# Performance work log

Measured on AMD Instinct MI355X. Metric: run time of the kernel, lower is better.

Reference implementation:

```python
import jax, jax.numpy as jnp
import numpy as np

# Model constants (from init_kwargs)
NF, NC, E, B = 100000, 4000, 500000, 256
D_FACT, D_COMP = 1536, 27
HIDDEN, HEADS, CPH = 128, 4, 32  # out_per_head = hidden // heads
NUM_LAYERS = 2
TIME_DIM = 8
T_SCALE = 30.0
EDGE_DIM = 2 + TIME_DIM  # [sentiment, decay, time2vec]
ATTN_SCALE = 1.0  # 1 / attn_temperature
NEG_SLOPE = 0.2


def time_edge_features(ea, lam):
    # ea: [E, 2] = [sentiment, decay]; second column in [0,1] -> decay branch
    s = jnp.clip(ea[:, 0:1], -1.0, 1.0)
    decay = jnp.clip(ea[:, 1:2], 0.0, 1.0)
    lam = jnp.maximum(lam, 1e-6)
    delta_t = -jnp.log(jnp.maximum(decay, 1e-6)) / lam
    t = jnp.log1p(jnp.maximum(delta_t, 0.0)) / T_SCALE  # [E,1]
    freqs = jnp.arange(1, TIME_DIM, dtype=ea.dtype)      # [TIME_DIM-1]
    sins = jnp.sin(t * freqs)                            # [E,TIME_DIM-1]
    return jnp.concatenate([s, decay, sins, t], axis=-1)  # [E, EDGE_DIM]


def seg_softmax(logits, seg, n):
    # logits: [E,H]; softmax over edges sharing the same destination node
    m = jax.ops.segment_max(logits, seg, num_segments=n)
    z = jnp.exp(logits - m[seg])
    den = jax.ops.segment_sum(z, seg, num_segments=n)
    return z / (den[seg] + 1e-16)


def seg_mean(x, seg, n):
    s = jax.ops.segment_sum(x, seg, num_segments=n)
    cnt = jax.ops.segment_sum(jnp.ones((x.shape[0],), x.dtype), seg, num_segments=n)
    return s / jnp.maximum(cnt, 1.0)[:, None]


def layernorm(x, g, b, eps=1e-5):
    mu = jnp.mean(x, axis=-1, keepdims=True)
    var = jnp.var(x, axis=-1, keepdims=True)
    return (x - mu) * jax.lax.rsqrt(var + eps) * g + b


def setup_inputs() -> dict:
    key = jax.random.key(0)
    ks = jax.random.split(key, 32)

    x_fact = jax.random.normal(ks[0], (NF, D_FACT), jnp.float32)
    x_company = jax.random.normal(ks[1], (NC, D_COMP), jnp.float32)
    u = jax.random.uniform(ks[2], (E, 2), jnp.float32)
    edge_attr = jnp.concatenate([u[:, 0:1] * 2.0 - 1.0, u[:, 1:2]], axis=1)
    edge_index = jnp.stack([
        jax.random.randint(ks[3], (E,), 0, NF),
        jax.random.randint(ks[4], (E,), 0, NC),
    ]).astype(jnp.int32)
    batch_fact = jnp.sort(jax.random.randint(ks[5], (NF,), 0, B)).astype(jnp.int32)
    batch_company = jnp.sort(jax.random.randint(ks[6], (NC,), 0, B)).astype(jnp.int32)

    def p(k, shape):
        return jax.random.normal(k, shape, jnp.float32) * 0.05

    inp = dict(
        x_fact=x_fact, x_company=x_company, edge_attr=edge_attr,
        edge_index=edge_index, batch_fact=batch_fact, batch_company=batch_company,
        lambda_decay=jnp.array(0.01, jnp.float32),
        Wf=p(ks[7], (D_FACT, HIDDEN)), bf=jnp.zeros((HIDDEN,), jnp.float32),
        Wc=p(ks[8], (D_COMP, HIDDEN)), bc=jnp.zeros((HIDDEN,), jnp.float32),
        Wl=p(ks[9], (NUM_LAYERS, HIDDEN, HIDDEN)), bl=jnp.zeros((NUM_LAYERS, HIDDEN), jnp.float32),
        Wr=p(ks[10], (NUM_LAYERS, HIDDEN, HIDDEN)), br=jnp.zeros((NUM_LAYERS, HIDDEN), jnp.float32),
        We=p(ks[11], (NUM_LAYERS, EDGE_DIM, HIDDEN)), be=jnp.zeros((NUM_LAYERS, HIDDEN), jnp.float32),
        att=p(ks[12], (NUM_LAYERS, HEADS, CPH)),
        bias_out=jnp.zeros((NUM_LAYERS, HIDDEN), jnp.float32),
        ln_g=jnp.ones((NUM_LAYERS, HIDDEN), jnp.float32), ln_b=jnp.zeros((NUM_LAYERS, HIDDEN), jnp.float32),
        Wg=p(ks[13], (2 * HIDDEN, 1)), bg=jnp.zeros((1,), jnp.float32),
        W1=p(ks[14], (HIDDEN, HIDDEN)), b1=jnp.zeros((HIDDEN,), jnp.float32),
        W2=p(ks[15], (HIDDEN, 1)), b2=jnp.zeros((1,), jnp.float32),
    )
    return inp


def reference(x_fact, x_company, edge_attr, edge_index, batch_fact, batch_company,
              lambda_decay, Wf, bf, Wc, bc, Wl, bl, Wr, br, We, be, att, bias_out,
              ln_g, ln_b, Wg, bg, W1, b1, W2, b2):
    src, dst = edge_index[0], edge_index[1]
    ef = time_edge_features(edge_attr, lambda_decay)          # [E, EDGE_DIM]

    # per-node-type input encoders
    hf = jax.nn.relu(x_fact @ Wf + bf)                         # [NF, H]
    hc = jax.nn.relu(x_company @ Wc + bc)                      # [NC, H]
    n_c = x_company.shape[0]

    for l in range(NUM_LAYERS):
        # GATv2 (edge-conditioned, bipartite fact->company, share_weights=False)
        gl = (hf @ Wl[l] + bl[l]).reshape(-1, HEADS, CPH)      # src transform [NF,H,C]
        gr = (hc @ Wr[l] + br[l]).reshape(-1, HEADS, CPH)      # dst transform [NC,H,C]
        ge = (ef @ We[l] + be[l]).reshape(-1, HEADS, CPH)      # edge transform [E,H,C]
        e = jax.nn.leaky_relu(gl[src] + gr[dst] + ge, NEG_SLOPE)  # [E,H,C]
        logits = jnp.einsum('ehc,hc->eh', e, att[l]) * ATTN_SCALE  # [E,H]
        alpha = seg_softmax(logits, dst, n_c)                   # scatter-softmax over dst
        msg = alpha[..., None] * gl[src]                        # [E,H,C]
        out = jax.ops.segment_sum(msg, dst, num_segments=n_c).reshape(n_c, HIDDEN) + bias_out[l]
        hc = layernorm(hc + jax.nn.relu(out), ln_g[l], ln_b[l])  # residual + post-norm

    # gated readout over graphs in batch
    pf = seg_mean(hf, batch_fact, B)                            # [B,H]
    pc = seg_mean(hc, batch_company, B)                         # [B,H]
    g = jax.nn.sigmoid(jnp.concatenate([pf, pc], axis=-1) @ Wg + bg)  # [B,1]
    h = g * pf + (1.0 - g) * pc                                 # [B,H]
    logit = jax.nn.relu(h @ W1 + b1) @ W2 + b2                  # [B,1]
    return logit
```

## Files before the change

### kernel.cpp

```cpp
#include <hip/hip_runtime.h>
#include <hip/hip_bf16.h>
#include <math.h>

#define NFAC 100000
#define NCOMP 4000
#define NEDGE 500000
#define NB 256
#define DF 1536
#define DC 27
#define H 128
#define EDIM 10
#define EDIMP 16

typedef __attribute__((ext_vector_type(8))) short short8v;
typedef __attribute__((ext_vector_type(4))) float f32x4;

#define GLOAD_LDS16(g, l)                                                              \
  __builtin_amdgcn_global_load_lds((const __attribute__((address_space(1))) unsigned int*)(g), \
                                   (__attribute__((address_space(3))) unsigned int*)(l), 16, 0, 0)

__device__ __forceinline__ float group32_sum(float v) {
#pragma unroll
  for (int m = 16; m > 0; m >>= 1) v += __shfl_xor(v, m);
  return v;
}

__device__ __forceinline__ unsigned short bf16rn(float x) {
  unsigned int u = __float_as_uint(x);
  unsigned int r = (u + 0x7fffu + ((u >> 16) & 1u)) >> 16;
  return (unsigned short)r;
}
__device__ __forceinline__ float bf16tof(unsigned short h) {
  return __uint_as_float(((unsigned int)h) << 16);
}

__global__ void k_edge_feat(const float* __restrict__ ea, const float* __restrict__ lamp,
                            float* __restrict__ ef) {
  int e = blockIdx.x * blockDim.x + threadIdx.x;
  if (e >= NEDGE) return;
  float s   = fminf(fmaxf(ea[2 * e], -1.f), 1.f);
  float dec = fminf(fmaxf(ea[2 * e + 1], 0.f), 1.f);
  float lam = fmaxf(lamp[0], 1e-6f);
  float dt  = -logf(fmaxf(dec, 1e-6f)) / lam;
  float t   = log1pf(fmaxf(dt, 0.f)) * (1.f / 30.f);
  float* o = ef + (size_t)e * EDIMP;
  o[0] = s;
  o[1] = dec;
#pragma unroll
  for (int k = 1; k < 8; k++) o[1 + k] = __sinf(t * (float)k);
  o[9] = t;
  o[10] = 0.f; o[11] = 0.f; o[12] = 0.f; o[13] = 0.f; o[14] = 0.f; o[15] = 0.f;
}

__global__ void k_hist(const int* __restrict__ dst, int* __restrict__ deg) {
  int e = blockIdx.x * blockDim.x + threadIdx.x;
  if (e < NEDGE) atomicAdd(&deg[dst[e]], 1);
}

__global__ __launch_bounds__(1024) void k_scan(const int* __restrict__ deg, int* __restrict__ off) {
  __shared__ int s[4096];
  int t = threadIdx.x;
  for (int i = t; i < 4096; i += 1024) s[i] = (i < NCOMP) ? deg[i] : 0;
  __syncthreads();
  for (int d = 1; d < 4096; d <<= 1) {
    int vals[4];
#pragma unroll
    for (int j = 0; j < 4; j++) {
      int i = t + j * 1024;
      vals[j] = (i >= d) ? s[i - d] : 0;
    }
    __syncthreads();
#pragma unroll
    for (int j = 0; j < 4; j++) {
      int i = t + j * 1024;
      s[i] += vals[j];
    }
    __syncthreads();
  }
  for (int i = t; i < 4096; i += 1024) off[i + 1] = s[i];
  if (t == 0) off[0] = 0;
}

__global__ void k_scatter(const int* __restrict__ dst, const int* __restrict__ src,
                          const int* __restrict__ off, int* __restrict__ cur,
                          int* __restrict__ eid, int* __restrict__ srcs) {
  int e = blockIdx.x * blockDim.x + threadIdx.x;
  if (e < NEDGE) {
    int d = dst[e];
    int p = atomicAdd(&cur[d], 1);
    eid[off[d] + p] = e;
    srcs[off[d] + p] = src[e];
  }
}

__global__ void k_conv_w(const float* __restrict__ W, unsigned short* __restrict__ Bh,
                         unsigned short* __restrict__ Bl, int K) {
  int i = blockIdx.x * blockDim.x + threadIdx.x;
  if (i >= K * H) return;
  int k = i >> 7, c = i & 127;
  float x = W[i];
  unsigned short h = bf16rn(x);
  unsigned short l = bf16rn(x - bf16tof(h));
  Bh[(size_t)c * K + k] = h;
  Bl[(size_t)c * K + k] = l;
}

__global__ void k_conv_wl2(const float* __restrict__ Wl, unsigned short* __restrict__ Bh,
                           unsigned short* __restrict__ Bl) {
  int i = blockIdx.x * blockDim.x + threadIdx.x;
  if (i >= 2 * H * H) return;
  int l = i >> 14;
  int r = i & 16383;
  int k = r >> 7, c = r & 127;
  float x = Wl[i];
  unsigned short h = bf16rn(x);
  unsigned short lo = bf16rn(x - bf16tof(h));
  int col = c + 128 * l;
  Bh[(size_t)col * H + k] = h;
  Bl[(size_t)col * H + k] = lo;
}

__device__ __forceinline__ unsigned int packhi(unsigned int u1, unsigned int u0) {
  return __builtin_amdgcn_perm(u1, u0, 0x07060302u);
}

__device__ __forceinline__ void split8(const float4& a0, const float4& a1, short8v& ah,
                                       short8v& al) {
  float xs[8] = {a0.x, a0.y, a0.z, a0.w, a1.x, a1.y, a1.z, a1.w};
  unsigned int hu[8], lu[8];
#pragma unroll
  for (int j = 0; j < 8; j++) {
    unsigned int u = __float_as_uint(xs[j]);
    hu[j] = u & 0xffff0000u;
    lu[j] = __float_as_uint(xs[j] - __uint_as_float(hu[j]));
  }
  unsigned int hw[4], lw[4];
#pragma unroll
  for (int j = 0; j < 4; j++) {
    hw[j] = packhi(hu[2 * j + 1], hu[2 * j]);
    lw[j] = packhi(lu[2 * j + 1], lu[2 * j]);
  }
  ah = *(short8v*)hw;
  al = *(short8v*)lw;
}

__global__ __launch_bounds__(256, 2) void k_gemm_mfma(const float* __restrict__ A,
                                                      const unsigned short* __restrict__ Bth,
                                                      const unsigned short* __restrict__ Btl,
                                                      const float* __restrict__ bias,
                                                      float* __restrict__ C, int M, int K,
                                                      int dorelu, float* __restrict__ Cpart) {
  __shared__ __align__(16) char smem[2][32768];
  int tid = threadIdx.x;
  int wave = tid >> 6, lane = tid & 63;
  int m0 = blockIdx.x * 128;
  int wm = (wave >> 1) * 64, wn = (wave & 1) * 64;
  int fr = lane & 15, fg = lane >> 4;
  int nsplit = gridDim.y;
  int Ks = K / nsplit;
  int kbeg = blockIdx.y * Ks;
  int nIter = Ks >> 5;

  f32x4 acc[4][4];
#pragma unroll
  for (int i = 0; i < 4; i++)
#pragma unroll
    for (int j = 0; j < 4; j++) acc[i][j] = (f32x4){0.f, 0.f, 0.f, 0.f};

  int a_row = (lane >> 3);
  int a_s = lane & 7;
  int b_col = (lane >> 2);
  int b_s = lane & 3;

  auto stage = [&](int buf, int k0) {
    char* base = smem[buf];
#pragma unroll
    for (int q = 0; q < 4; q++) {
      int j = wave + 4 * q;
      int row = j * 8 + a_row;
      int grow = m0 + row;
      if (grow >= M) grow = 0;
      const float* src = A + (size_t)grow * K + k0 + ((a_s ^ (row & 7)) << 2);
      GLOAD_LDS16(src, base + j * 1024);
    }
#pragma unroll
    for (int q = 0; q < 2; q++) {
      int j = wave + 4 * q;
      int col = j * 16 + b_col;
      int soff = k0 + ((b_s ^ (col & 3)) << 3);
      GLOAD_LDS16(Bth + (size_t)col * K + soff, base + 16384 + j * 1024);
      GLOAD_LDS16(Btl + (size_t)col * K + soff, base + 24576 + j * 1024);
    }
  };

  stage(0, kbeg);
  __syncthreads();

  for (int it = 0; it < nIter; ++it) {
    int cur = it & 1;
    if (it + 1 < nIter) stage(cur ^ 1, kbeg + ((it + 1) << 5));
    const char* cb = smem[cur];
    short8v ah[4], al[4];
#pragma unroll
    for (int mf = 0; mf < 4; mf++) {
      int r = wm + 16 * mf + fr;
      int s0 = (2 * fg) ^ (r & 7);
      int s1 = (2 * fg + 1) ^ (r & 7);
      float4 a0 = *(const float4*)(cb + r * 128 + s0 * 16);
      float4 a1 = *(const float4*)(cb + r * 128 + s1 * 16);
      split8(a0, a1, ah[mf], al[mf]);
    }
#pragma unroll
    for (int nf = 0; nf < 4; nf++) {
      int c = wn + 16 * nf + fr;
      int sb = fg ^ (c & 3);
      short8v bh = *(const short8v*)(cb + 16384 + c * 64 + sb * 16);
      short8v bl = *(const short8v*)(cb + 24576 + c * 64 + sb * 16);
#pragma unroll
      for (int mf = 0; mf < 4; mf++) {
        acc[mf][nf] = __builtin_amdgcn_mfma_f32_16x16x32_bf16(ah[mf], bh, acc[mf][nf], 0, 0, 0);
        acc[mf][nf] = __builtin_amdgcn_mfma_f32_16x16x32_bf16(ah[mf], bl, acc[mf][nf], 0, 0, 0);
        acc[mf][nf] = __builtin_amdgcn_mfma_f32_16x16x32_bf16(al[mf], bh, acc[mf][nf], 0, 0, 0);
      }
    }
    __syncthreads();
  }

  if (nsplit == 1) {
#pragma unroll
    for (int mf = 0; mf < 4; mf++) {
      int rbase = m0 + wm + 16 * mf + 4 * fg;
#pragma unroll
      for (int nf = 0; nf < 4; nf++) {
        int col = wn + 16 * nf + fr;
        float bv = bias[col];
#pragma unroll
        for (int j = 0; j < 4; j++) {
          int row = rbase + j;
          if (row < M) {
            float v = acc[mf][nf][j] + bv;
            if (dorelu) v = fmaxf(v, 0.f);
            C[(size_t)row * H + col] = v;
          }
        }
      }
    }
  } else {
    float* P = Cpart + (size_t)blockIdx.y * M * H;
#pragma unroll
    for (int mf = 0; mf < 4; mf++) {
      int rbase = m0 + wm + 16 * mf + 4 * fg;
#pragma unroll
      for (int nf = 0; nf < 4; nf++) {
        int col = wn + 16 * nf + fr;
#pragma unroll
        for (int j = 0; j < 4; j++) {
          int row = rbase + j;
          if (row < M) P[(size_t)row * H + col] = acc[mf][nf][j];
        }
      }
    }
  }
}

__global__ __launch_bounds__(256, 2) void k_gemm_n256(const float* __restrict__ A,
                                                      const unsigned short* __restrict__ Bth,
                                                      const unsigned short* __restrict__ Btl,
                                                      const float* __restrict__ bias,
                                                      float* __restrict__ C, int M) {
  __shared__ __align__(16) char smem[2][40960];
  const int K = 128;
  int tid = threadIdx.x;
  int wave = tid >> 6, lane = tid & 63;
  int m0 = blockIdx.x * 64;
  int wn = wave * 64;
  int fr = lane & 15, fg = lane >> 4;

  f32x4 acc[4][4];
#pragma unroll
  for (int i = 0; i < 4; i++)
#pragma unroll
    for (int j = 0; j < 4; j++) acc[i][j] = (f32x4){0.f, 0.f, 0.f, 0.f};

  int a_row = (lane >> 3);
  int a_s = lane & 7;
  int b_col = (lane >> 2);
  int b_s = lane & 3;

  auto stage = [&](int buf, int k0) {
    char* base = smem[buf];
#pragma unroll
    for (int q = 0; q < 2; q++) {
      int j = wave + 4 * q;
      int row = j * 8 + a_row;
      int grow = m0 + row;
      if (grow >= M) grow = 0;
      GLOAD_LDS16(A + (size_t)grow * K + k0 + ((a_s ^ (row & 7)) << 2), base + j * 1024);
    }
#pragma unroll
    for (int q = 0; q < 4; q++) {
      int j = wave + 4 * q;
      int col = j * 16 + b_col;
      int soff = k0 + ((b_s ^ (col & 3)) << 3);
      GLOAD_LDS16(Bth + (size_t)col * K + soff, base + 8192 + j * 1024);
      GLOAD_LDS16(Btl + (size_t)col * K + soff, base + 24576 + j * 1024);
    }
  };

  stage(0, 0);
  __syncthreads();

  for (int it = 0; it < 4; ++it) {
    int cur = it & 1;
    if (it + 1 < 4) stage(cur ^ 1, (it + 1) << 5);
    const char* cb = smem[cur];
    short8v ah[4], al[4];
#pragma unroll
    for (int mf = 0; mf < 4; mf++) {
      int r = 16 * mf + fr;
      int s0 = (2 * fg) ^ (r & 7);
      int s1 = (2 * fg + 1) ^ (r & 7);
      float4 a0 = *(const float4*)(cb + r * 128 + s0 * 16);
      float4 a1 = *(const float4*)(cb + r * 128 + s1 * 16);
      split8(a0, a1, ah[mf], al[mf]);
    }
#pragma unroll
    for (int nf = 0; nf < 4; nf++) {
      int c = wn + 16 * nf + fr;
      int sb = fg ^ (c & 3);
      short8v bh = *(const short8v*)(cb + 8192 + c * 64 + sb * 16);
      short8v bl = *(const short8v*)(cb + 24576 + c * 64 + sb * 16);
#pragma unroll
      for (int mf = 0; mf < 4; mf++) {
        acc[mf][nf] = __builtin_amdgcn_mfma_f32_16x16x32_bf16(ah[mf], bh, acc[mf][nf], 0, 0, 0);
        acc[mf][nf] = __builtin_amdgcn_mfma_f32_16x16x32_bf16(ah[mf], bl, acc[mf][nf], 0, 0, 0);
        acc[mf][nf] = __builtin_amdgcn_mfma_f32_16x16x32_bf16(al[mf], bh, acc[mf][nf], 0, 0, 0);
      }
    }
    __syncthreads();
  }

#pragma unroll
  for (int mf = 0; mf < 4; mf++) {
    int rbase = m0 + 16 * mf + 4 * fg;
#pragma unroll
    for (int nf = 0; nf < 4; nf++) {
      int col = wn + 16 * nf + fr;
      float bv = bias[col];
#pragma unroll
      for (int j = 0; j < 4; j++) {
        int row = rbase + j;
        if (row < M) C[(size_t)row * 256 + col] = acc[mf][nf][j] + bv;
      }
    }
  }
}

__global__ __launch_bounds__(256) void k_reduce2(const float* __restrict__ P0,
                                                 const float* __restrict__ P1,
                                                 const float* __restrict__ bias,
                                                 float* __restrict__ C, int total4) {
  int i = blockIdx.x * blockDim.x + threadIdx.x;
  if (i >= total4) return;
  float4 a = ((const float4*)P0)[i];
  float4 b = ((const float4*)P1)[i];
  float4 bv = ((const float4*)bias)[i & 31];
  float4 r;
  r.x = fmaxf(a.x + b.x + bv.x, 0.f);
  r.y = fmaxf(a.y + b.y + bv.y, 0.f);
  r.z = fmaxf(a.z + b.z + bv.z, 0.f);
  r.w = fmaxf(a.w + b.w + bv.w, 0.f);
  ((float4*)C)[i] = r;
}

__global__ void k_enc_comp(const float* __restrict__ X, const float* __restrict__ Wc,
                           const float* __restrict__ bc, float* __restrict__ hc) {
  int tid = threadIdx.x;
  int r = blockIdx.x * 2 + (tid >> 7);
  int j = tid & 127;
  if (r >= NCOMP) return;
  float acc = bc[j];
  const float* x = X + (size_t)r * DC;
#pragma unroll
  for (int k = 0; k < DC; k++) acc = fmaf(x[k], Wc[k * H + j], acc);
  hc[(size_t)r * H + j] = fmaxf(acc, 0.f);
}

__global__ __launch_bounds__(128) void k_node(
    const float* __restrict__ gl, const float* __restrict__ ef, const int* __restrict__ srcs,
    const int* __restrict__ csr_off, const int* __restrict__ csr_eid,
    const float* __restrict__ Wr, const float* __restrict__ br, const float* __restrict__ We,
    const float* __restrict__ be, const float* __restrict__ att,
    const float* __restrict__ bias_out, const float* __restrict__ lng,
    const float* __restrict__ lnb, float* __restrict__ hc) {
  int v = blockIdx.x;
  int t = threadIdx.x;
  __shared__ float hcs[H];
  __shared__ float red[2], redq[2];
  float x = hc[(size_t)v * H + t];
  hcs[t] = x;
  float wre[EDIM];
#pragma unroll
  for (int k = 0; k < EDIM; k++) wre[k] = We[k * H + t];
  float attv = att[t];
  float bev = be[t];
  __syncthreads();
  float grv = br[t];
  for (int k = 0; k < H; k++) grv = fmaf(hcs[k], Wr[k * H + t], grv);
  float grb = grv + bev;

  int e0 = csr_off[v], e1 = csr_off[v + 1];
  float m = -INFINITY, s = 0.f, acc = 0.f;
  int i = e0;
  float glv = 0.f;
  float4 f0 = {0, 0, 0, 0}, f1 = {0, 0, 0, 0};
  float2 f2 = {0, 0};
  if (i < e1) {
    int eid = csr_eid[i];
    int sid = srcs[i];
    glv = gl[(size_t)sid * 256 + t];
    const float* efr = ef + (size_t)eid * EDIMP;
    f0 = *(const float4*)(efr);
    f1 = *(const float4*)(efr + 4);
    f2 = *(const float2*)(efr + 8);
  }
  while (i < e1) {
    int ni = i + 1;
    float nglv = 0.f;
    float4 nf0 = {0, 0, 0, 0}, nf1 = {0, 0, 0, 0};
    float2 nf2 = {0, 0};
    if (ni < e1) {
      int eid = csr_eid[ni];
      int sid = srcs[ni];
      nglv = gl[(size_t)sid * 256 + t];
      const float* efr = ef + (size_t)eid * EDIMP;
      nf0 = *(const float4*)(efr);
      nf1 = *(const float4*)(efr + 4);
      nf2 = *(const float2*)(efr + 8);
    }
    float ge = grb;
    ge = fmaf(f0.x, wre[0], ge);
    ge = fmaf(f0.y, wre[1], ge);
    ge = fmaf(f0.z, wre[2], ge);
    ge = fmaf(f0.w, wre[3], ge);
    ge = fmaf(f1.x, wre[4], ge);
    ge = fmaf(f1.y, wre[5], ge);
    ge = fmaf(f1.z, wre[6], ge);
    ge = fmaf(f1.w, wre[7], ge);
    ge = fmaf(f2.x, wre[8], ge);
    ge = fmaf(f2.y, wre[9], ge);
    float ev = glv + ge;
    ev = ev > 0.f ? ev : 0.2f * ev;
    float logit = group32_sum(ev * attv);
    if (logit > m) {
      float scale = __expf(m - logit);
      s = s * scale + 1.f;
      acc = acc * scale + glv;
      m = logit;
    } else {
      float z = __expf(logit - m);
      s += z;
      acc = fmaf(z, glv, acc);
    }
    glv = nglv;
    f0 = nf0;
    f1 = nf1;
    f2 = nf2;
    i = ni;
  }
  float outv = acc / (s + 1e-16f);
  outv += bias_out[t];
  outv = fmaxf(outv, 0.f);
  float y = x + outv;
  float sv = y, qv = y * y;
#pragma unroll
  for (int mm = 32; mm > 0; mm >>= 1) {
    sv += __shfl_xor(sv, mm);
    qv += __shfl_xor(qv, mm);
  }
  int wid = t >> 6, lane = t & 63;
  if (lane == 0) {
    red[wid] = sv;
    redq[wid] = qv;
  }
  __syncthreads();
  float mean = (red[0] + red[1]) * (1.f / H);
  float var = (redq[0] + redq[1]) * (1.f / H) - mean * mean;
  float r = rsqrtf(var + 1e-5f);
  hc[(size_t)v * H + t] = (y - mean) * r * lng[t] + lnb[t];
}

template <int CHUNK>
__global__ __launch_bounds__(128) void k_segmean(const float* __restrict__ X,
                                                 const int* __restrict__ seg, int n,
                                                 float* __restrict__ sum, int* __restrict__ cnt) {
  int t = threadIdx.x;
  int n0 = blockIdx.x * CHUNK;
  int n1 = min(n0 + CHUNK, n);
  float acc = 0.f;
  int c = 0;
  int curs = -1;
  for (int i = n0; i < n1; ++i) {
    int sg = seg[i];
    if (sg != curs) {
      if (curs >= 0) {
        atomicAdd(&sum[(size_t)curs * H + t], acc);
        if (t == 0) atomicAdd(&cnt[curs], c);
      }
      curs = sg;
      acc = 0.f;
      c = 0;
    }
    acc += X[(size_t)i * H + t];
    c++;
  }
  if (curs >= 0) {
    atomicAdd(&sum[(size_t)curs * H + t], acc);
    if (t == 0) atomicAdd(&cnt[curs], c);
  }
}

__global__ __launch_bounds__(128) void k_readout(const float* __restrict__ pf,
                                                 const float* __restrict__ pc,
                                                 const int* __restrict__ cf,
                                                 const int* __restrict__ cc,
                                                 const float* __restrict__ Wg,
                                                 const float* __restrict__ bg,
                                                 const float* __restrict__ W1,
                                                 const float* __restrict__ b1,
                                                 const float* __restrict__ W2,
                                                 const float* __restrict__ b2,
                                                 float* __restrict__ out) {
  int b = blockIdx.x, t = threadIdx.x;
  __shared__ float hs[H];
  __shared__ float red[2], red2[2];
  int wid = t >> 6, lane = t & 63;
  float nf = fmaxf((float)cf[b], 1.f);
  float nc = fmaxf((float)cc[b], 1.f);
  float pfv = pf[(size_t)b * H + t] / nf;
  float pcv = pc[(size_t)b * H + t] / nc;
  float gp = pfv * Wg[t] + pcv * Wg[H + t];
  float sv = gp;
#pragma unroll
  for (int mm = 32; mm > 0; mm >>= 1) sv += __shfl_xor(sv, mm);
  if (lane == 0) red[wid] = sv;
  __syncthreads();
  float g = 1.f / (1.f + expf(-(red[0] + red[1] + bg[0])));
  float h = g * pfv + (1.f - g) * pcv;
  hs[t] = h;
  __syncthreads();
  float a = b1[t];
  for (int k = 0; k < H; k++) a = fmaf(hs[k], W1[k * H + t], a);
  a = fmaxf(a, 0.f);
  float p = a * W2[t];
#pragma unroll
  for (int mm = 32; mm > 0; mm >>= 1) p += __shfl_xor(p, mm);
  if (lane == 0) red2[wid] = p;
  __syncthreads();
  if (t == 0) out[b] = red2[0] + red2[1] + b2[0];
}

extern "C" void kernel_launch(void* const* d_in, const int* in_sizes, int n_in, void* d_out,
                              int out_size, void* d_ws, size_t ws_size, hipStream_t stream) {
  const float* x_fact = (const float*)d_in[0];
  const float* x_comp = (const float*)d_in[1];
  const float* ea = (const float*)d_in[2];
  const int* eidx = (const int*)d_in[3];
  const int* batf = (const int*)d_in[4];
  const int* batc = (const int*)d_in[5];
  const float* lam = (const float*)d_in[6];
  const float* Wf = (const float*)d_in[7];
  const float* bf = (const float*)d_in[8];
  const float* Wc = (const float*)d_in[9];
  const float* bc = (const float*)d_in[10];
  const float* Wl = (const float*)d_in[11];
  const float* bl = (const float*)d_in[12];
  const float* Wr = (const float*)d_in[13];
  const float* br_ = (const float*)d_in[14];
  const float* We = (const float*)d_in[15];
  const float* be = (const float*)d_in[16];
  const float* att = (const float*)d_in[17];
  const float* b_out = (const float*)d_in[18];
  const float* lng = (const float*)d_in[19];
  const float* lnb = (const float*)d_in[20];
  const float* Wg = (const float*)d_in[21];
  const float* bg = (const float*)d_in[22];
  const float* W1 = (const float*)d_in[23];
  const float* b1 = (const float*)d_in[24];
  const float* W2 = (const float*)d_in[25];
  const float* b2 = (const float*)d_in[26];
  float* out = (float*)d_out;

  char* w = (char*)d_ws;
  auto carve = [&](size_t bytes) -> char* {
    char* p = w;
    w += (bytes + 255) & ~(size_t)255;
    return p;
  };
  float* HF = (float*)carve((size_t)NFAC * H * 4);
  float* GL = (float*)carve((size_t)NFAC * H * 4);
  float* CP1 = (float*)carve((size_t)NFAC * H * 4);
  float* GL2 = GL;
  float* HC = (float*)carve((size_t)NCOMP * H * 4);
  float* EF = (float*)carve((size_t)NEDGE * EDIMP * 4);
  int* OFF = (int*)carve(4100 * 4);
  int* EID = (int*)carve((size_t)NEDGE * 4);
  int* SRCS = (int*)carve((size_t)NEDGE * 4);
  unsigned short* WfH = (unsigned short*)carve((size_t)DF * H * 2);
  unsigned short* WfL = (unsigned short*)carve((size_t)DF * H * 2);
  unsigned short* WlH2 = (unsigned short*)carve((size_t)256 * H * 2);
  unsigned short* WlL2 = (unsigned short*)carve((size_t)256 * H * 2);
  char* zbase = w;
  int* DEG = (int*)carve(4096 * 4);
  int* CUR = (int*)carve(4096 * 4);
  float* PF = (float*)carve((size_t)NB * H * 4);
  float* PC = (float*)carve((size_t)NB * H * 4);
  int* CF = (int*)carve(NB * 4);
  int* CC = (int*)carve(NB * 4);
  size_t zbytes = (size_t)(w - zbase);
  hipMemsetAsync(zbase, 0, zbytes, stream);

  const int* srcArr = eidx;
  const int* dstArr = eidx + NEDGE;

  k_edge_feat<<<(NEDGE + 255) / 256, 256, 0, stream>>>(ea, lam, EF);
  k_hist<<<(NEDGE + 255) / 256, 256, 0, stream>>>(dstArr, DEG);
  k_scan<<<1, 1024, 0, stream>>>(DEG, OFF);
  k_scatter<<<(NEDGE + 255) / 256, 256, 0, stream>>>(dstArr, srcArr, OFF, CUR, EID, SRCS);

  k_conv_w<<<(DF * H + 255) / 256, 256, 0, stream>>>(Wf, WfH, WfL, DF);
  k_conv_wl2<<<(2 * H * H + 255) / 256, 256, 0, stream>>>(Wl, WlH2, WlL2);

  {
    float* CPART = GL;
    dim3 grid((NFAC + 127) / 128, 2);
    k_gemm_mfma<<<grid, 256, 0, stream>>>(x_fact, WfH, WfL, bf, HF, NFAC, DF, 1, CPART);
    int total4 = NFAC * H / 4;
    k_reduce2<<<(total4 + 255) / 256, 256, 0, stream>>>(GL, CP1, bf, HF, total4);
  }
  k_enc_comp<<<NCOMP / 2, 256, 0, stream>>>(x_comp, Wc, bc, HC);

  k_gemm_n256<<<(NFAC + 63) / 64, 256, 0, stream>>>(HF, WlH2, WlL2, bl, GL2, NFAC);

  for (int l = 0; l < 2; l++) {
    k_node<<<NCOMP, 128, 0, stream>>>(GL2 + l * 128, EF, SRCS, OFF, EID,
                                      Wr + (size_t)l * H * H, br_ + l * H,
                                      We + (size_t)l * EDIM * H, be + l * H, att + l * H,
                                      b_out + l * H, lng + l * H, lnb + l * H, HC);
  }

  k_segmean<128><<<(NFAC + 127) / 128, 128, 0, stream>>>(HF, batf, NFAC, PF, CF);
  k_segmean<64><<<(NCOMP + 63) / 64, 128, 0, stream>>>(HC, batc, NCOMP, PC, CC);
  k_readout<<<NB, 128, 0, stream>>>(PF, PC, CF, CC, Wg, bg, W1, b1, W2, b2, out);
}
```

Before: 734.9 us.

## Store layer-2 source transform in fp16 and simplify edge-loop prefetch

The N=256 GEMM output (gl for the second layer, read by gather in the node kernel) is now written as fp16 instead of fp32, halving the bytes written and gathered per edge. The node kernel's software pipelining is reduced to prefetching only the edge and source indices, with the gl and edge-feature loads issued at the top of each iteration. This trades some numerical precision in attention logits and messages, and possibly latency hiding, for less memory traffic.

```diff
diff --git a/kernel.cpp b/kernel.cpp
--- a/kernel.cpp
+++ b/kernel.cpp
@@ -1,5 +1,6 @@
 #include <hip/hip_runtime.h>
 #include <hip/hip_bf16.h>
+#include <hip/hip_fp16.h>
 #include <math.h>
 
 #define NFAC 100000
@@ -267,7 +268,7 @@
                                                       const unsigned short* __restrict__ Bth,
                                                       const unsigned short* __restrict__ Btl,
                                                       const float* __restrict__ bias,
-                                                      float* __restrict__ C, int M) {
+                                                      __half* __restrict__ C, int M) {
   __shared__ __align__(16) char smem[2][40960];
   const int K = 128;
   int tid = threadIdx.x;
@@ -350,7 +351,7 @@
 #pragma unroll
       for (int j = 0; j < 4; j++) {
         int row = rbase + j;
-        if (row < M) C[(size_t)row * 256 + col] = acc[mf][nf][j] + bv;
+        if (row < M) C[(size_t)row * 256 + col] = __float2half(acc[mf][nf][j] + bv);
       }
     }
   }
@@ -387,7 +388,7 @@
 }
 
 __global__ __launch_bounds__(128) void k_node(
-    const float* __restrict__ gl, const float* __restrict__ ef, const int* __restrict__ srcs,
+    const __half* __restrict__ gl, const float* __restrict__ ef, const int* __restrict__ srcs,
     const int* __restrict__ csr_off, const int* __restrict__ csr_eid,
     const float* __restrict__ Wr, const float* __restrict__ br, const float* __restrict__ We,
     const float* __restrict__ be, const float* __restrict__ att,
@@ -412,31 +413,21 @@
   int e0 = csr_off[v], e1 = csr_off[v + 1];
   float m = -INFINITY, s = 0.f, acc = 0.f;
   int i = e0;
-  float glv = 0.f;
-  float4 f0 = {0, 0, 0, 0}, f1 = {0, 0, 0, 0};
-  float2 f2 = {0, 0};
+  int eid = 0, sid = 0;
   if (i < e1) {
-    int eid = csr_eid[i];
-    int sid = srcs[i];
-    glv = gl[(size_t)sid * 256 + t];
+    eid = csr_eid[i];
+    sid = srcs[i];
+  }
+  while (i < e1) {
+    float glv = __half2float(gl[(size_t)sid * 256 + t]);
     const float* efr = ef + (size_t)eid * EDIMP;
-    f0 = *(const float4*)(efr);
-    f1 = *(const float4*)(efr + 4);
-    f2 = *(const float2*)(efr + 8);
-  }
-  while (i < e1) {
+    float4 f0 = *(const float4*)(efr);
+    float4 f1 = *(const float4*)(efr + 4);
+    float2 f2 = *(const float2*)(efr + 8);
     int ni = i + 1;
-    float nglv = 0.f;
-    float4 nf0 = {0, 0, 0, 0}, nf1 = {0, 0, 0, 0};
-    float2 nf2 = {0, 0};
     if (ni < e1) {
-      int eid = csr_eid[ni];
-      int sid = srcs[ni];
-      nglv = gl[(size_t)sid * 256 + t];
-      const float* efr = ef + (size_t)eid * EDIMP;
-      nf0 = *(const float4*)(efr);
-      nf1 = *(const float4*)(efr + 4);
-      nf2 = *(const float2*)(efr + 8);
+      eid = csr_eid[ni];
+      sid = srcs[ni];
     }
     float ge = grb;
     ge = fmaf(f0.x, wre[0], ge);
@@ -462,10 +453,6 @@
       s += z;
       acc = fmaf(z, glv, acc);
     }
-    glv = nglv;
-    f0 = nf0;
-    f1 = nf1;
-    f2 = nf2;
     i = ni;
   }
   float outv = acc / (s + 1e-16f);
@@ -600,7 +587,7 @@
   float* HF = (float*)carve((size_t)NFAC * H * 4);
   float* GL = (float*)carve((size_t)NFAC * H * 4);
   float* CP1 = (float*)carve((size_t)NFAC * H * 4);
-  float* GL2 = GL;
+  __half* GL2 = (__half*)GL;
   float* HC = (float*)carve((size_t)NCOMP * H * 4);
   float* EF = (float*)carve((size_t)NEDGE * EDIMP * 4);
   int* OFF = (int*)carve(4100 * 4);
```

Result: faster. 692.4 us (-5.8%).
